# Optimization experiments

Measured on AMD Instinct MI355X. Metric: run time of the kernel, lower is better.

The kernel has to match this reference:

```python
import jax, jax.numpy as jnp
import numpy as np
from jax import lax

V, E, C_OUT, K, NTAGS = 32000, 256, 256, 3, 32
B, T = 64, 2048


def setup_inputs() -> dict:
    key = jax.random.key(0)
    ks = jax.random.split(key, 12)
    inputs = jax.random.randint(ks[0], (B, T), 0, V)
    emb_table = jax.random.normal(ks[1], (V, E), jnp.float32) * 0.02
    emb_table = emb_table.at[1].set(0.0)  # padding_idx=1
    conv1_w = jax.random.normal(ks[2], (C_OUT, E, K), jnp.float32) * 0.02
    conv1_b = jax.random.normal(ks[3], (C_OUT,), jnp.float32) * 0.02
    conv2_w = jax.random.normal(ks[4], (C_OUT, C_OUT, K), jnp.float32) * 0.02
    conv2_b = jax.random.normal(ks[5], (C_OUT,), jnp.float32) * 0.02
    fc_w = jax.random.normal(ks[6], (NTAGS, E), jnp.float32) * 0.02
    fc_b = jax.random.normal(ks[7], (NTAGS,), jnp.float32) * 0.02
    trans = jax.random.normal(ks[8], (NTAGS, NTAGS), jnp.float32) * 0.1
    start_t = jax.random.normal(ks[9], (NTAGS,), jnp.float32) * 0.1
    end_t = jax.random.normal(ks[10], (NTAGS,), jnp.float32) * 0.1
    return {"inputs": inputs, "emb_table": emb_table,
            "conv1_w": conv1_w, "conv1_b": conv1_b,
            "conv2_w": conv2_w, "conv2_b": conv2_b,
            "fc_w": fc_w, "fc_b": fc_b,
            "trans": trans, "start_t": start_t, "end_t": end_t}


def _conv1d(x, w, b):
    # x: [B, C_in, T], w: [C_out, C_in, K], padding=1
    y = lax.conv_general_dilated(x, w, window_strides=(1,), padding=[(1, 1)],
                                 dimension_numbers=("NCH", "OIH", "NCH"))
    return y + b[None, :, None]


def _crf_log_partition(emissions, trans, start_t, end_t):
    # emissions: [B, T, NTAGS] -> logZ per sequence [B]
    em_t = jnp.swapaxes(emissions, 0, 1)  # [T, B, NTAGS]
    alpha0 = start_t[None, :] + em_t[0]   # [B, NTAGS]

    def step(alpha, emit):
        # alpha: [B, C]; broadcast prev-tag x next-tag: [B, C, C]
        scores = alpha[:, :, None] + trans[None, :, :] + emit[:, None, :]
        new_alpha = jax.scipy.special.logsumexp(scores, axis=1)
        return new_alpha, None

    alpha, _ = lax.scan(step, alpha0, em_t[1:])
    return jax.scipy.special.logsumexp(alpha + end_t[None, :], axis=-1)


def reference(inputs, emb_table, conv1_w, conv1_b, conv2_w, conv2_b,
              fc_w, fc_b, trans, start_t, end_t):
    emb = emb_table[inputs]                    # [B, T, E]
    x = jnp.swapaxes(emb, 1, 2)                # [B, E, T]
    x = _conv1d(x, conv1_w, conv1_b)           # [B, C, T]
    x = _conv1d(x, conv2_w, conv2_b)           # [B, C, T]
    h = jnp.swapaxes(x, 1, 2)                  # [B, T, E]  (dropout = identity in eval)
    logits = jnp.einsum("bte,ce->btc", h, fc_w) + fc_b  # [B, T, NTAGS]
    return _crf_log_partition(logits, trans, start_t, end_t)  # [B]
```

## Files before the change

### kernel.cpp

```cpp
#include <hip/hip_runtime.h>
#include <hip/hip_bf16.h>

typedef float f32x4 __attribute__((ext_vector_type(4)));
typedef __bf16 bf16x8 __attribute__((ext_vector_type(8)));
typedef __bf16 bf16x4 __attribute__((ext_vector_type(4)));

__global__ __launch_bounds__(256) void transpose_w(const float* __restrict__ w1,
                                                   const float* __restrict__ w2,
                                                   float* __restrict__ w1t,
                                                   float* __restrict__ w2t) {
  int tid = blockIdx.x * 256 + threadIdx.x;
  if (tid < 196608) {
    float v = w1[tid];
    int k1 = tid % 3;
    int r = tid / 3;
    int e = r & 255;
    int cp = r >> 8;
    w1t[(k1 * 256 + e) * 256 + cp] = v;
  } else {
    int t2 = tid - 196608;
    float v = w2[t2];
    int k2 = t2 % 3;
    int r = t2 / 3;
    int cp = r & 255;
    int c = r >> 8;
    w2t[(k2 * 256 + cp) * 256 + c] = v;
  }
}

__global__ __launch_bounds__(256) void prep_g(const float* __restrict__ fcw,
                                              const float* __restrict__ w2t,
                                              float* __restrict__ G) {
  int tid = blockIdx.x * 256 + threadIdx.x;
  int cp = tid & 255;
  int rest = tid >> 8;
  int n = rest & 31;
  int k2 = rest >> 5;
  const float* wr = w2t + (k2 * 256 + cp) * 256;
  const float* fr = fcw + n * 256;
  float acc = 0.f;
  #pragma unroll 8
  for (int c = 0; c < 256; c += 4) {
    f32x4 a = *(const f32x4*)(fr + c);
    f32x4 bb = *(const f32x4*)(wr + c);
    acc = fmaf(a[0], bb[0], acc); acc = fmaf(a[1], bb[1], acc);
    acc = fmaf(a[2], bb[2], acc); acc = fmaf(a[3], bb[3], acc);
  }
  G[(k2 * 32 + n) * 256 + cp] = acc;
}

__global__ __launch_bounds__(256) void prep_wf(const float* __restrict__ G,
                                               const float* __restrict__ w1t,
                                               const float* __restrict__ b1,
                                               const float* __restrict__ b2,
                                               const float* __restrict__ fcw,
                                               const float* __restrict__ fcb,
                                               __bf16* __restrict__ wfb,
                                               float* __restrict__ C0,
                                               float* __restrict__ CT,
                                               float* __restrict__ bias_tot,
                                               float* __restrict__ c0v,
                                               float* __restrict__ cTv) {
  int tid = blockIdx.x * 256 + threadIdx.x;
  if (tid < 40960) {
    int n = tid & 31;
    int r = tid >> 5;
    int kk = r % 5;
    int e = r / 5;
    float acc = 0.f;
    #pragma unroll
    for (int k2 = 0; k2 < 3; ++k2) {
      int k1 = kk - k2;
      if (k1 < 0 || k1 > 2) continue;
      const float* g = G + (k2 * 32 + n) * 256;
      const float* wr = w1t + (k1 * 256 + e) * 256;
      #pragma unroll 8
      for (int cp = 0; cp < 256; cp += 4) {
        f32x4 a = *(const f32x4*)(g + cp);
        f32x4 bb = *(const f32x4*)(wr + cp);
        acc = fmaf(a[0], bb[0], acc); acc = fmaf(a[1], bb[1], acc);
        acc = fmaf(a[2], bb[2], acc); acc = fmaf(a[3], bb[3], acc);
      }
    }
    int j = kk * 32 + n;
    int jt = j >> 4, jl = j & 15;
    int et = e >> 5, el = e & 31;
    int lane = jl | ((el >> 3) << 4);
    int rr = el & 7;
    wfb[((jt * 8 + et) * 64 + lane) * 8 + rr] = (__bf16)acc;
  } else if (tid < 57344) {
    int t2 = tid - 40960;
    int which = (t2 >= 8192);
    if (which) t2 -= 8192;
    int n = t2 & 31;
    int e = t2 >> 5;
    const float* g = G + ((which ? 2 : 0) * 32 + n) * 256;
    int k1 = which ? 0 : 2;
    const float* wr = w1t + (k1 * 256 + e) * 256;
    float acc = 0.f;
    #pragma unroll 8
    for (int cp = 0; cp < 256; cp += 4) {
      f32x4 a = *(const f32x4*)(g + cp);
      f32x4 bb = *(const f32x4*)(wr + cp);
      acc = fmaf(a[0], bb[0], acc); acc = fmaf(a[1], bb[1], acc);
      acc = fmaf(a[2], bb[2], acc); acc = fmaf(a[3], bb[3], acc);
    }
    (which ? CT : C0)[n * 256 + e] = acc;
  } else if (tid < 57376) {
    int n = tid - 57344;
    float bt = fcb[n];
    for (int c = 0; c < 256; ++c) bt = fmaf(fcw[n * 256 + c], b2[c], bt);
    float s0 = 0.f, s1 = 0.f, s2 = 0.f;
    const float* g0 = G + (0 * 32 + n) * 256;
    const float* g1 = G + (1 * 32 + n) * 256;
    const float* g2 = G + (2 * 32 + n) * 256;
    for (int cp = 0; cp < 256; ++cp) {
      s0 = fmaf(g0[cp], b1[cp], s0);
      s1 = fmaf(g1[cp], b1[cp], s1);
      s2 = fmaf(g2[cp], b1[cp], s2);
    }
    bias_tot[n] = bt + s0 + s1 + s2;
    c0v[n] = s0;
    cTv[n] = s2;
  }
}

__global__ __launch_bounds__(256) void ptab_corr(const float* __restrict__ emb,
                                                 const __bf16* __restrict__ wfb,
                                                 __bf16* __restrict__ P,
                                                 const int* __restrict__ idx,
                                                 const float* __restrict__ C0,
                                                 const float* __restrict__ CT,
                                                 const float* __restrict__ c0v,
                                                 const float* __restrict__ cTv,
                                                 float* __restrict__ corr) {
  __shared__ float red[256];
  if (blockIdx.x < 500) {
    int lane = threadIdx.x & 63;
    int mt = blockIdx.x * 4 + (threadIdx.x >> 6);
    int ln = lane & 15;
    int q = lane >> 4;
    int m = mt * 16 + ln;
    f32x4 acc[10];
    #pragma unroll
    for (int jt = 0; jt < 10; ++jt) acc[jt] = (f32x4){0.f, 0.f, 0.f, 0.f};
    const float* arow = emb + m * 256 + q * 8;
    #pragma unroll
    for (int et = 0; et < 8; ++et) {
      f32x4 a0 = *(const f32x4*)(arow + et * 32);
      f32x4 a1 = *(const f32x4*)(arow + et * 32 + 4);
      bf16x8 af;
      af[0] = (__bf16)a0[0]; af[1] = (__bf16)a0[1];
      af[2] = (__bf16)a0[2]; af[3] = (__bf16)a0[3];
      af[4] = (__bf16)a1[0]; af[5] = (__bf16)a1[1];
      af[6] = (__bf16)a1[2]; af[7] = (__bf16)a1[3];
      #pragma unroll
      for (int jt = 0; jt < 10; ++jt) {
        bf16x8 bfr = *(const bf16x8*)(wfb + ((jt * 8 + et) * 64 + lane) * 8);
        acc[jt] = __builtin_amdgcn_mfma_f32_16x16x32_bf16(af, bfr, acc[jt], 0, 0, 0);
      }
    }
    #pragma unroll
    for (int jt = 0; jt < 10; ++jt) {
      __bf16* pp = P + (mt * 16 + q * 4) * 160 + jt * 16 + ln;
      pp[0]   = (__bf16)acc[jt][0];
      pp[160] = (__bf16)acc[jt][1];
      pp[320] = (__bf16)acc[jt][2];
      pp[480] = (__bf16)acc[jt][3];
    }
  } else {
    int bid = blockIdx.x - 500;
    int b = bid >> 1;
    int which = bid & 1;
    int n = threadIdx.x & 31;
    int part = threadIdx.x >> 5;
    int v = idx[b * 2048 + (which ? 2047 : 0)];
    const float* C = which ? CT : C0;
    const float* er = emb + v * 256 + part * 32;
    const float* cr = C + n * 256 + part * 32;
    float s = 0.f;
    #pragma unroll
    for (int e = 0; e < 32; ++e) s = fmaf(cr[e], er[e], s);
    red[threadIdx.x] = s;
    __syncthreads();
    if (part == 0) {
      float tot = (which ? cTv : c0v)[n];
      #pragma unroll
      for (int p = 0; p < 8; ++p) tot += red[p * 32 + n];
      corr[(which * 64 + b) * 32 + n] = tot;
    }
  }
}

__global__ __launch_bounds__(256) void logits_k(const int* __restrict__ idx,
                                                const __bf16* __restrict__ P,
                                                const float* __restrict__ bias_tot,
                                                const float* __restrict__ corr,
                                                __bf16* __restrict__ L) {
  int tid = blockIdx.x * 256 + threadIdx.x;
  int q = tid & 7;
  int tp = (tid >> 3) & 1023;
  int b = tid >> 13;
  int t0 = tp * 2;
  const int* ib = idx + b * 2048;
  f32x4 bias = *(const f32x4*)(bias_tot + q * 4);
  f32x4 acc0 = bias, acc1 = bias;
  #pragma unroll
  for (int j = 0; j < 6; ++j) {
    int tt = t0 + j - 2;
    if (tt < 0 || tt > 2047) continue;
    int v = ib[tt];
    const __bf16* pr = P + v * 160 + q * 4;
    if (j < 5) {
      bf16x4 pv = *(const bf16x4*)(pr + j * 32);
      acc0[0] += (float)pv[0]; acc0[1] += (float)pv[1];
      acc0[2] += (float)pv[2]; acc0[3] += (float)pv[3];
    }
    if (j >= 1) {
      bf16x4 pv = *(const bf16x4*)(pr + (j - 1) * 32);
      acc1[0] += (float)pv[0]; acc1[1] += (float)pv[1];
      acc1[2] += (float)pv[2]; acc1[3] += (float)pv[3];
    }
  }
  if (t0 == 0)        acc0 -= *(const f32x4*)(corr + b * 32 + q * 4);
  if (t0 + 1 == 2047) acc1 -= *(const f32x4*)(corr + (64 + b) * 32 + q * 4);
  bf16x4 r0, r1;
  r0[0] = (__bf16)(__expf(acc0[0]) * 0.03125f);
  r0[1] = (__bf16)(__expf(acc0[1]) * 0.03125f);
  r0[2] = (__bf16)(__expf(acc0[2]) * 0.03125f);
  r0[3] = (__bf16)(__expf(acc0[3]) * 0.03125f);
  r1[0] = (__bf16)(__expf(acc1[0]) * 0.03125f);
  r1[1] = (__bf16)(__expf(acc1[1]) * 0.03125f);
  r1[2] = (__bf16)(__expf(acc1[2]) * 0.03125f);
  r1[3] = (__bf16)(__expf(acc1[3]) * 0.03125f);
  __bf16* Lb = L + (b * 2048 + t0) * 32 + q * 4;
  *(bf16x4*)(Lb) = r0;
  *(bf16x4*)(Lb + 32) = r1;
}

__global__ __launch_bounds__(256) void crf_stage1(const __bf16* __restrict__ Lexp,
                                                  const float* __restrict__ trans,
                                                  __bf16* __restrict__ PcB) {
  __shared__ __bf16 sl[4][32 * 40];
  int lane = threadIdx.x & 63;
  int w = threadIdx.x >> 6;
  int chain = blockIdx.x * 4 + w;
  int c = chain >> 6;
  int b = chain & 63;
  int ln = lane & 15;
  int q = lane >> 4;
  float tA0[8], tA1[8];
  #pragma unroll
  for (int e = 0; e < 8; ++e) {
    tA0[e] = __expf(trans[(q * 8 + e) * 32 + ln]);
    tA1[e] = __expf(trans[(q * 8 + e) * 32 + 16 + ln]);
  }
  bf16x8 bf0, bf1;
  #pragma unroll
  for (int e = 0; e < 8; ++e) {
    int k = q * 8 + e;
    bf0[e] = (k == ln) ? (__bf16)1.0f : (__bf16)0.0f;
    bf1[e] = (k == 16 + ln) ? (__bf16)1.0f : (__bf16)0.0f;
  }
  int tstart = c * 32 + 1;
  int total = (c == 63) ? 31 : 32;
  const __bf16* Le = Lexp + (b * 2048 + tstart) * 32;
  __bf16* myS = &sl[w][0];

  auto step = [&](float sc0, float sc1) {
    bf16x8 a0, a1;
    #pragma unroll
    for (int e = 0; e < 8; ++e) {
      a0[e] = (__bf16)(sc0 * tA0[e]);
      a1[e] = (__bf16)(sc1 * tA1[e]);
    }
    f32x4 z = {0.f, 0.f, 0.f, 0.f};
    f32x4 c00 = __builtin_amdgcn_mfma_f32_16x16x32_bf16(a0, bf0, z, 0, 0, 0);
    f32x4 c01 = __builtin_amdgcn_mfma_f32_16x16x32_bf16(a0, bf1, z, 0, 0, 0);
    f32x4 c10 = __builtin_amdgcn_mfma_f32_16x16x32_bf16(a1, bf0, z, 0, 0, 0);
    f32x4 c11 = __builtin_amdgcn_mfma_f32_16x16x32_bf16(a1, bf1, z, 0, 0, 0);
    bf16x4 w00, w01, w10, w11;
    #pragma unroll
    for (int r = 0; r < 4; ++r) {
      w00[r] = (__bf16)c00[r]; w01[r] = (__bf16)c01[r];
      w10[r] = (__bf16)c10[r]; w11[r] = (__bf16)c11[r];
    }
    *(bf16x4*)(myS + (ln) * 40      + q * 4)      = w00;
    *(bf16x4*)(myS + (16 + ln) * 40 + q * 4)      = w01;
    *(bf16x4*)(myS + (ln) * 40      + 16 + q * 4) = w10;
    *(bf16x4*)(myS + (16 + ln) * 40 + 16 + q * 4) = w11;
    bf0 = *(const bf16x8*)(myS + (ln) * 40 + q * 8);
    bf1 = *(const bf16x8*)(myS + (16 + ln) * 40 + q * 8);
  };

  float s0[8], s1[8];
  #pragma unroll
  for (int i = 0; i < 8; ++i) {
    s0[i] = (float)Le[i * 32 + ln];
    s1[i] = (float)Le[i * 32 + 16 + ln];
  }
  int nbatch = total >> 3;
  int rem = total & 7;
  for (int bt = 0; bt < nbatch; ++bt) {
    float n0[8], n1[8];
    bool more = (bt + 1 < nbatch) || (rem != 0 && bt + 1 == nbatch);
    if (more) {
      int bs = (bt + 1) * 8;
      #pragma unroll
      for (int i = 0; i < 8; ++i) {
        int k = bs + i; if (k >= total) k = total - 1;
        n0[i] = (float)Le[k * 32 + ln];
        n1[i] = (float)Le[k * 32 + 16 + ln];
      }
    }
    #pragma unroll
    for (int s = 0; s < 8; ++s) step(s0[s], s1[s]);
    #pragma unroll
    for (int i = 0; i < 8; ++i) { s0[i] = n0[i]; s1[i] = n1[i]; }
  }
  if (rem) {
    #pragma unroll
    for (int s = 0; s < 7; ++s) step(s0[s], s1[s]);
  }
  bf16x8 o0, o1;
  #pragma unroll
  for (int e = 0; e < 8; ++e) {
    o0[e] = myS[(q * 8 + e) * 40 + ln];
    o1[e] = myS[(q * 8 + e) * 40 + 16 + ln];
  }
  __bf16* dst = PcB + ((b * 64 + c) * 64 + lane) * 16;
  *(bf16x8*)(dst)     = o0;
  *(bf16x8*)(dst + 8) = o1;
}

__global__ __launch_bounds__(512) void crf_tail(const __bf16* __restrict__ Lexp,
                                                const __bf16* __restrict__ PcB,
                                                const float* __restrict__ start_t,
                                                const float* __restrict__ end_t,
                                                float* __restrict__ out) {
  __shared__ float sg[8][1024];
  __shared__ __bf16 sl[8][32 * 40];
  int b = blockIdx.x;
  int tid = threadIdx.x;
  int lane = tid & 63;
  int g = tid >> 6;
  int ln = lane & 15;
  int q = lane >> 4;
  const __bf16* base = PcB + ((b * 64 + g * 8) * 64) * 16;
  bf16x8 a0 = *(const bf16x8*)(base + lane * 16);
  bf16x8 a1 = *(const bf16x8*)(base + lane * 16 + 8);
  bf16x8 bf0, bf1;
  #pragma unroll
  for (int e = 0; e < 8; ++e) {
    int k = q * 8 + e;
    bf0[e] = (k == ln) ? (__bf16)1.0f : (__bf16)0.0f;
    bf1[e] = (k == 16 + ln) ? (__bf16)1.0f : (__bf16)0.0f;
  }
  __bf16* myS = &sl[g][0];
  f32x4 c00, c01, c10, c11;
  for (int j = 0; j < 8; ++j) {
    bf16x8 na0, na1;
    if (j < 7) {
      const __bf16* nb = base + (j + 1) * 1024 + lane * 16;
      na0 = *(const bf16x8*)(nb);
      na1 = *(const bf16x8*)(nb + 8);
    }
    f32x4 z = {0.f, 0.f, 0.f, 0.f};
    c00 = __builtin_amdgcn_mfma_f32_16x16x32_bf16(a0, bf0, z, 0, 0, 0);
    c01 = __builtin_amdgcn_mfma_f32_16x16x32_bf16(a0, bf1, z, 0, 0, 0);
    c10 = __builtin_amdgcn_mfma_f32_16x16x32_bf16(a1, bf0, z, 0, 0, 0);
    c11 = __builtin_amdgcn_mfma_f32_16x16x32_bf16(a1, bf1, z, 0, 0, 0);
    if (j < 7) {
      bf16x4 w00, w01, w10, w11;
      #pragma unroll
      for (int r = 0; r < 4; ++r) {
        w00[r] = (__bf16)c00[r]; w01[r] = (__bf16)c01[r];
        w10[r] = (__bf16)c10[r]; w11[r] = (__bf16)c11[r];
      }
      *(bf16x4*)(myS + (ln) * 40      + q * 4)      = w00;
      *(bf16x4*)(myS + (16 + ln) * 40 + q * 4)      = w01;
      *(bf16x4*)(myS + (ln) * 40      + 16 + q * 4) = w10;
      *(bf16x4*)(myS + (16 + ln) * 40 + 16 + q * 4) = w11;
      bf0 = *(const bf16x8*)(myS + (ln) * 40 + q * 8);
      bf1 = *(const bf16x8*)(myS + (16 + ln) * 40 + q * 8);
      a0 = na0; a1 = na1;
    }
  }
  #pragma unroll
  for (int r = 0; r < 4; ++r) {
    sg[g][(ln) * 32      + q * 4 + r]      = c00[r];
    sg[g][(16 + ln) * 32 + q * 4 + r]      = c01[r];
    sg[g][(ln) * 32      + 16 + q * 4 + r] = c10[r];
    sg[g][(16 + ln) * 32 + 16 + q * 4 + r] = c11[r];
  }
  int j2 = tid & 31;
  float u = __expf(start_t[j2]) * (float)Lexp[b * 2048 * 32 + j2] * 32.f;
  __syncthreads();
  float logacc = 0.f;
  #pragma unroll
  for (int gg = 0; gg < 8; ++gg) {
    const float* M = &sg[gg][0];
    float nu0 = 0.f, nu1 = 0.f, nu2 = 0.f, nu3 = 0.f;
    #pragma unroll
    for (int k = 0; k < 32; k += 4) {
      nu0 = fmaf(__shfl(u, k,     32), M[(k)     * 32 + j2], nu0);
      nu1 = fmaf(__shfl(u, k + 1, 32), M[(k + 1) * 32 + j2], nu1);
      nu2 = fmaf(__shfl(u, k + 2, 32), M[(k + 2) * 32 + j2], nu2);
      nu3 = fmaf(__shfl(u, k + 3, 32), M[(k + 3) * 32 + j2], nu3);
    }
    float nu = (nu0 + nu1) + (nu2 + nu3);
    float ssum = nu;
    #pragma unroll
    for (int o = 1; o < 32; o <<= 1) ssum += __shfl_xor(ssum, o, 32);
    u = nu * __builtin_amdgcn_rcpf(ssum);
    logacc += __logf(ssum);
  }
  float term = u * __expf(end_t[j2]);
  #pragma unroll
  for (int o = 1; o < 32; o <<= 1) term += __shfl_xor(term, o, 32);
  if (tid == 0)
    out[b] = logacc + logf(term) + (float)(2047.0 * 5.0 * 0.69314718055994530942);
}

extern "C" void kernel_launch(void* const* d_in, const int* in_sizes, int n_in,
                              void* d_out, int out_size, void* d_ws, size_t ws_size,
                              hipStream_t stream) {
  const int*   idx  = (const int*)d_in[0];
  const float* emb  = (const float*)d_in[1];
  const float* w1   = (const float*)d_in[2];
  const float* b1   = (const float*)d_in[3];
  const float* w2   = (const float*)d_in[4];
  const float* b2   = (const float*)d_in[5];
  const float* fcw  = (const float*)d_in[6];
  const float* fcb  = (const float*)d_in[7];
  const float* trn  = (const float*)d_in[8];
  const float* st   = (const float*)d_in[9];
  const float* en   = (const float*)d_in[10];

  char* ws = (char*)d_ws;
  __bf16* P     = (__bf16*)(ws + 0);
  __bf16* L     = (__bf16*)(ws + 10240000);
  __bf16* PcB   = (__bf16*)(ws + 18628608);
  float*  w1t   = (float*)(ws + 27017216);
  float*  w2t   = (float*)(ws + 27803648);
  __bf16* WfB   = (__bf16*)(ws + 43794432);
  float*  G     = (float*)(ws + 43876352);
  float*  C0    = (float*)(ws + 43974656);
  float*  CT    = (float*)(ws + 44007424);
  float*  bias  = (float*)(ws + 44040192);
  float*  c0v   = (float*)(ws + 44040320);
  float*  cTv   = (float*)(ws + 44040448);
  float*  corr  = (float*)(ws + 44040576);

  transpose_w<<<1536, 256, 0, stream>>>(w1, w2, w1t, w2t);
  prep_g     <<<96,   256, 0, stream>>>(fcw, w2t, G);
  prep_wf    <<<225,  256, 0, stream>>>(G, w1t, b1, b2, fcw, fcb, WfB, C0, CT, bias, c0v, cTv);
  ptab_corr  <<<628,  256, 0, stream>>>(emb, WfB, P, idx, C0, CT, c0v, cTv, corr);
  logits_k   <<<2048, 256, 0, stream>>>(idx, P, bias, corr, L);
  crf_stage1 <<<1024, 256, 0, stream>>>(L, trn, PcB);
  crf_tail   <<<64,   512, 0, stream>>>(L, PcB, st, en, (float*)d_out);
}
```

Measured before the change: 186.6 us.

## Drop weight transpose kernel; stage raw conv weights in shared memory for prep

Removes the separate transpose_w kernel and its w1t/w2t workspace buffers. prep_g and prep_wf now load slices of the original conv weights straight into LDS and compute from there, with two accumulators per dot product. This saves one launch and the global round-trip of transposed weights. The cost is far fewer blocks (32 instead of 96/225), so the prep kernels have much less parallelism, and the bias block is serialized onto block 0.

```diff
diff --git a/kernel.cpp b/kernel.cpp
--- a/kernel.cpp
+++ b/kernel.cpp
@@ -5,52 +5,37 @@
 typedef __bf16 bf16x8 __attribute__((ext_vector_type(8)));
 typedef __bf16 bf16x4 __attribute__((ext_vector_type(4)));
 
-__global__ __launch_bounds__(256) void transpose_w(const float* __restrict__ w1,
-                                                   const float* __restrict__ w2,
-                                                   float* __restrict__ w1t,
-                                                   float* __restrict__ w2t) {
-  int tid = blockIdx.x * 256 + threadIdx.x;
-  if (tid < 196608) {
-    float v = w1[tid];
-    int k1 = tid % 3;
-    int r = tid / 3;
-    int e = r & 255;
-    int cp = r >> 8;
-    w1t[(k1 * 256 + e) * 256 + cp] = v;
-  } else {
-    int t2 = tid - 196608;
-    float v = w2[t2];
-    int k2 = t2 % 3;
-    int r = t2 / 3;
-    int cp = r & 255;
-    int c = r >> 8;
-    w2t[(k2 * 256 + cp) * 256 + c] = v;
-  }
-}
-
 __global__ __launch_bounds__(256) void prep_g(const float* __restrict__ fcw,
-                                              const float* __restrict__ w2t,
+                                              const float* __restrict__ w2,
                                               float* __restrict__ G) {
-  int tid = blockIdx.x * 256 + threadIdx.x;
-  int cp = tid & 255;
-  int rest = tid >> 8;
-  int n = rest & 31;
-  int k2 = rest >> 5;
-  const float* wr = w2t + (k2 * 256 + cp) * 256;
-  const float* fr = fcw + n * 256;
-  float acc = 0.f;
-  #pragma unroll 8
-  for (int c = 0; c < 256; c += 4) {
-    f32x4 a = *(const f32x4*)(fr + c);
-    f32x4 bb = *(const f32x4*)(wr + c);
-    acc = fmaf(a[0], bb[0], acc); acc = fmaf(a[1], bb[1], acc);
-    acc = fmaf(a[2], bb[2], acc); acc = fmaf(a[3], bb[3], acc);
-  }
-  G[(k2 * 32 + n) * 256 + cp] = acc;
+  __shared__ float s[256 * 24];
+  int cp0 = blockIdx.x * 8;
+  for (int l = threadIdx.x; l < 256 * 24; l += 256) {
+    int c = l / 24, r = l - c * 24;
+    s[l] = w2[c * 768 + cp0 * 3 + r];
+  }
+  __syncthreads();
+  #pragma unroll
+  for (int o = 0; o < 3; ++o) {
+    int oid = threadIdx.x + o * 256;
+    int cpl = oid & 7;
+    int p = oid >> 3;
+    int n = p & 31, k2 = p >> 5;
+    const float* fr = fcw + n * 256;
+    float a0 = 0.f, a1 = 0.f;
+    for (int c = 0; c < 256; c += 4) {
+      f32x4 a = *(const f32x4*)(fr + c);
+      a0 = fmaf(a[0], s[(c + 0) * 24 + cpl * 3 + k2], a0);
+      a1 = fmaf(a[1], s[(c + 1) * 24 + cpl * 3 + k2], a1);
+      a0 = fmaf(a[2], s[(c + 2) * 24 + cpl * 3 + k2], a0);
+      a1 = fmaf(a[3], s[(c + 3) * 24 + cpl * 3 + k2], a1);
+    }
+    G[(k2 * 32 + n) * 256 + cp0 + cpl] = a0 + a1;
+  }
 }
 
 __global__ __launch_bounds__(256) void prep_wf(const float* __restrict__ G,
-                                               const float* __restrict__ w1t,
+                                               const float* __restrict__ w1,
                                                const float* __restrict__ b1,
                                                const float* __restrict__ b2,
                                                const float* __restrict__ fcw,
@@ -61,53 +46,65 @@
                                                float* __restrict__ bias_tot,
                                                float* __restrict__ c0v,
                                                float* __restrict__ cTv) {
-  int tid = blockIdx.x * 256 + threadIdx.x;
-  if (tid < 40960) {
-    int n = tid & 31;
-    int r = tid >> 5;
-    int kk = r % 5;
-    int e = r / 5;
+  __shared__ float s[256 * 24];
+  int e0 = blockIdx.x * 8;
+  for (int l = threadIdx.x; l < 256 * 24; l += 256) {
+    int cp = l / 24, r = l - cp * 24;
+    s[l] = w1[cp * 768 + e0 * 3 + r];
+  }
+  __syncthreads();
+  #pragma unroll
+  for (int o = 0; o < 5; ++o) {
+    int oid = threadIdx.x + o * 256;
+    int el = oid / 160;
+    int rem = oid - el * 160;
+    int kk = rem >> 5;
+    int n = rem & 31;
+    int e = e0 + el;
     float acc = 0.f;
     #pragma unroll
     for (int k2 = 0; k2 < 3; ++k2) {
       int k1 = kk - k2;
       if (k1 < 0 || k1 > 2) continue;
       const float* g = G + (k2 * 32 + n) * 256;
-      const float* wr = w1t + (k1 * 256 + e) * 256;
-      #pragma unroll 8
+      float a0 = 0.f, a1 = 0.f;
       for (int cp = 0; cp < 256; cp += 4) {
-        f32x4 a = *(const f32x4*)(g + cp);
-        f32x4 bb = *(const f32x4*)(wr + cp);
-        acc = fmaf(a[0], bb[0], acc); acc = fmaf(a[1], bb[1], acc);
-        acc = fmaf(a[2], bb[2], acc); acc = fmaf(a[3], bb[3], acc);
+        f32x4 gv = *(const f32x4*)(g + cp);
+        a0 = fmaf(gv[0], s[(cp + 0) * 24 + el * 3 + k1], a0);
+        a1 = fmaf(gv[1], s[(cp + 1) * 24 + el * 3 + k1], a1);
+        a0 = fmaf(gv[2], s[(cp + 2) * 24 + el * 3 + k1], a0);
+        a1 = fmaf(gv[3], s[(cp + 3) * 24 + el * 3 + k1], a1);
       }
+      acc += a0 + a1;
     }
     int j = kk * 32 + n;
     int jt = j >> 4, jl = j & 15;
-    int et = e >> 5, el = e & 31;
-    int lane = jl | ((el >> 3) << 4);
-    int rr = el & 7;
+    int et = e >> 5, el2 = e & 31;
+    int lane = jl | ((el2 >> 3) << 4);
+    int rr = el2 & 7;
     wfb[((jt * 8 + et) * 64 + lane) * 8 + rr] = (__bf16)acc;
-  } else if (tid < 57344) {
-    int t2 = tid - 40960;
-    int which = (t2 >= 8192);
-    if (which) t2 -= 8192;
-    int n = t2 & 31;
-    int e = t2 >> 5;
+  }
+  #pragma unroll
+  for (int o = 0; o < 2; ++o) {
+    int oid = threadIdx.x + o * 256;
+    int which = oid >> 8;
+    int el = (oid >> 5) & 7;
+    int n = oid & 31;
+    int e = e0 + el;
+    int k1 = which ? 0 : 2;
     const float* g = G + ((which ? 2 : 0) * 32 + n) * 256;
-    int k1 = which ? 0 : 2;
-    const float* wr = w1t + (k1 * 256 + e) * 256;
-    float acc = 0.f;
-    #pragma unroll 8
+    float a0 = 0.f, a1 = 0.f;
     for (int cp = 0; cp < 256; cp += 4) {
-      f32x4 a = *(const f32x4*)(g + cp);
-      f32x4 bb = *(const f32x4*)(wr + cp);
-      acc = fmaf(a[0], bb[0], acc); acc = fmaf(a[1], bb[1], acc);
-      acc = fmaf(a[2], bb[2], acc); acc = fmaf(a[3], bb[3], acc);
-    }
-    (which ? CT : C0)[n * 256 + e] = acc;
-  } else if (tid < 57376) {
-    int n = tid - 57344;
+      f32x4 gv = *(const f32x4*)(g + cp);
+      a0 = fmaf(gv[0], s[(cp + 0) * 24 + el * 3 + k1], a0);
+      a1 = fmaf(gv[1], s[(cp + 1) * 24 + el * 3 + k1], a1);
+      a0 = fmaf(gv[2], s[(cp + 2) * 24 + el * 3 + k1], a0);
+      a1 = fmaf(gv[3], s[(cp + 3) * 24 + el * 3 + k1], a1);
+    }
+    (which ? CT : C0)[n * 256 + e] = a0 + a1;
+  }
+  if (blockIdx.x == 0 && threadIdx.x < 32) {
+    int n = threadIdx.x;
     float bt = fcb[n];
     for (int c = 0; c < 256; ++c) bt = fmaf(fcw[n * 256 + c], b2[c], bt);
     float s0 = 0.f, s1 = 0.f, s2 = 0.f;
@@ -441,22 +438,19 @@
   __bf16* P     = (__bf16*)(ws + 0);
   __bf16* L     = (__bf16*)(ws + 10240000);
   __bf16* PcB   = (__bf16*)(ws + 18628608);
-  float*  w1t   = (float*)(ws + 27017216);
-  float*  w2t   = (float*)(ws + 27803648);
-  __bf16* WfB   = (__bf16*)(ws + 43794432);
-  float*  G     = (float*)(ws + 43876352);
-  float*  C0    = (float*)(ws + 43974656);
-  float*  CT    = (float*)(ws + 44007424);
-  float*  bias  = (float*)(ws + 44040192);
-  float*  c0v   = (float*)(ws + 44040320);
-  float*  cTv   = (float*)(ws + 44040448);
-  float*  corr  = (float*)(ws + 44040576);
-
-  transpose_w<<<1536, 256, 0, stream>>>(w1, w2, w1t, w2t);
-  prep_g     <<<96,   256, 0, stream>>>(fcw, w2t, G);
-  prep_wf    <<<225,  256, 0, stream>>>(G, w1t, b1, b2, fcw, fcb, WfB, C0, CT, bias, c0v, cTv);
-  ptab_corr  <<<628,  256, 0, stream>>>(emb, WfB, P, idx, C0, CT, c0v, cTv, corr);
-  logits_k   <<<2048, 256, 0, stream>>>(idx, P, bias, corr, L);
-  crf_stage1 <<<1024, 256, 0, stream>>>(L, trn, PcB);
-  crf_tail   <<<64,   512, 0, stream>>>(L, PcB, st, en, (float*)d_out);
-}
+  __bf16* WfB   = (__bf16*)(ws + 27017216);
+  float*  G     = (float*)(ws + 27099136);
+  float*  C0    = (float*)(ws + 27197440);
+  float*  CT    = (float*)(ws + 27230208);
+  float*  bias  = (float*)(ws + 27262976);
+  float*  c0v   = (float*)(ws + 27263104);
+  float*  cTv   = (float*)(ws + 27263232);
+  float*  corr  = (float*)(ws + 27263360);
+
+  prep_g    <<<32,   256, 0, stream>>>(fcw, w2, G);
+  prep_wf   <<<32,   256, 0, stream>>>(G, w1, b1, b2, fcw, fcb, WfB, C0, CT, bias, c0v, cTv);
+  ptab_corr <<<628,  256, 0, stream>>>(emb, WfB, P, idx, C0, CT, c0v, cTv, corr);
+  logits_k  <<<2048, 256, 0, stream>>>(idx, P, bias, corr, L);
+  crf_stage1<<<1024, 256, 0, stream>>>(L, trn, PcB);
+  crf_tail  <<<64,   512, 0, stream>>>(L, PcB, st, en, (float*)d_out);
+}
```

Result: slower. 254.6 us (+36.4%).

## Fuse CRF tail into stage1 via last-block atomic counter per sequence

Applied to the files above, without the earlier changes.

Removes the separate crf_tail launch. Each crf_stage1 block now bumps a per-sequence atomic counter after writing its chunk products, and the block that finishes last for a sequence combines that sequence's chunk matrices and computes the final log-partition. The counters are zeroed in prep_g, and workspace offsets are compacted to make room for them. This saves a kernel launch and the tail's serial dependency on the whole stage, at the cost of threadfence/atomic overhead and the combine matrices being held in bf16 instead of fp32 in shared memory.

```diff
diff --git a/kernel.cpp b/kernel.cpp
--- a/kernel.cpp
+++ b/kernel.cpp
@@ -30,7 +30,9 @@
 
 __global__ __launch_bounds__(256) void prep_g(const float* __restrict__ fcw,
                                               const float* __restrict__ w2t,
-                                              float* __restrict__ G) {
+                                              float* __restrict__ G,
+                                              int* __restrict__ cnt) {
+  if (blockIdx.x == 0 && threadIdx.x < 64) cnt[threadIdx.x] = 0;
   int tid = blockIdx.x * 256 + threadIdx.x;
   int cp = tid & 255;
   int rest = tid >> 8;
@@ -240,8 +242,14 @@
 
 __global__ __launch_bounds__(256) void crf_stage1(const __bf16* __restrict__ Lexp,
                                                   const float* __restrict__ trans,
-                                                  __bf16* __restrict__ PcB) {
+                                                  __bf16* __restrict__ PcB,
+                                                  const float* __restrict__ start_t,
+                                                  const float* __restrict__ end_t,
+                                                  int* __restrict__ cnt,
+                                                  float* __restrict__ out) {
   __shared__ __bf16 sl[4][32 * 40];
+  __shared__ __bf16 sgB[8][1024];
+  __shared__ int winb[4];
   int lane = threadIdx.x & 63;
   int w = threadIdx.x >> 6;
   int chain = blockIdx.x * 4 + w;
@@ -331,95 +339,102 @@
   __bf16* dst = PcB + ((b * 64 + c) * 64 + lane) * 16;
   *(bf16x8*)(dst)     = o0;
   *(bf16x8*)(dst + 8) = o1;
-}
-
-__global__ __launch_bounds__(512) void crf_tail(const __bf16* __restrict__ Lexp,
-                                                const __bf16* __restrict__ PcB,
-                                                const float* __restrict__ start_t,
-                                                const float* __restrict__ end_t,
-                                                float* __restrict__ out) {
-  __shared__ float sg[8][1024];
-  __shared__ __bf16 sl[8][32 * 40];
-  int b = blockIdx.x;
-  int tid = threadIdx.x;
-  int lane = tid & 63;
-  int g = tid >> 6;
-  int ln = lane & 15;
-  int q = lane >> 4;
-  const __bf16* base = PcB + ((b * 64 + g * 8) * 64) * 16;
-  bf16x8 a0 = *(const bf16x8*)(base + lane * 16);
-  bf16x8 a1 = *(const bf16x8*)(base + lane * 16 + 8);
-  bf16x8 bf0, bf1;
-  #pragma unroll
-  for (int e = 0; e < 8; ++e) {
-    int k = q * 8 + e;
-    bf0[e] = (k == ln) ? (__bf16)1.0f : (__bf16)0.0f;
-    bf1[e] = (k == 16 + ln) ? (__bf16)1.0f : (__bf16)0.0f;
-  }
-  __bf16* myS = &sl[g][0];
-  f32x4 c00, c01, c10, c11;
-  for (int j = 0; j < 8; ++j) {
-    bf16x8 na0, na1;
-    if (j < 7) {
-      const __bf16* nb = base + (j + 1) * 1024 + lane * 16;
-      na0 = *(const bf16x8*)(nb);
-      na1 = *(const bf16x8*)(nb + 8);
-    }
-    f32x4 z = {0.f, 0.f, 0.f, 0.f};
-    c00 = __builtin_amdgcn_mfma_f32_16x16x32_bf16(a0, bf0, z, 0, 0, 0);
-    c01 = __builtin_amdgcn_mfma_f32_16x16x32_bf16(a0, bf1, z, 0, 0, 0);
-    c10 = __builtin_amdgcn_mfma_f32_16x16x32_bf16(a1, bf0, z, 0, 0, 0);
-    c11 = __builtin_amdgcn_mfma_f32_16x16x32_bf16(a1, bf1, z, 0, 0, 0);
-    if (j < 7) {
-      bf16x4 w00, w01, w10, w11;
+
+  __threadfence();
+  __syncthreads();
+  if (threadIdx.x < 4) {
+    int myb = ((blockIdx.x * 4) & 63) + threadIdx.x;
+    int old = atomicAdd(&cnt[myb], 1);
+    winb[threadIdx.x] = (old == 63) ? myb : -1;
+  }
+  __syncthreads();
+
+  for (int s = 0; s < 4; ++s) {
+    int wb = winb[s];
+    if (wb < 0) continue;
+    __threadfence();
+    #pragma unroll
+    for (int half = 0; half < 2; ++half) {
+      int g = w + half * 4;
+      const __bf16* base = PcB + ((wb * 64 + g * 8) * 64) * 16;
+      bf16x8 a0 = *(const bf16x8*)(base + lane * 16);
+      bf16x8 a1 = *(const bf16x8*)(base + lane * 16 + 8);
+      bf16x8 tb0, tb1;
+      #pragma unroll
+      for (int e = 0; e < 8; ++e) {
+        int k = q * 8 + e;
+        tb0[e] = (k == ln) ? (__bf16)1.0f : (__bf16)0.0f;
+        tb1[e] = (k == 16 + ln) ? (__bf16)1.0f : (__bf16)0.0f;
+      }
+      f32x4 d00, d01, d10, d11;
+      for (int j = 0; j < 8; ++j) {
+        bf16x8 na0, na1;
+        if (j < 7) {
+          const __bf16* nb = base + (j + 1) * 1024 + lane * 16;
+          na0 = *(const bf16x8*)(nb);
+          na1 = *(const bf16x8*)(nb + 8);
+        }
+        f32x4 z = {0.f, 0.f, 0.f, 0.f};
+        d00 = __builtin_amdgcn_mfma_f32_16x16x32_bf16(a0, tb0, z, 0, 0, 0);
+        d01 = __builtin_amdgcn_mfma_f32_16x16x32_bf16(a0, tb1, z, 0, 0, 0);
+        d10 = __builtin_amdgcn_mfma_f32_16x16x32_bf16(a1, tb0, z, 0, 0, 0);
+        d11 = __builtin_amdgcn_mfma_f32_16x16x32_bf16(a1, tb1, z, 0, 0, 0);
+        if (j < 7) {
+          bf16x4 w00, w01, w10, w11;
+          #pragma unroll
+          for (int r = 0; r < 4; ++r) {
+            w00[r] = (__bf16)d00[r]; w01[r] = (__bf16)d01[r];
+            w10[r] = (__bf16)d10[r]; w11[r] = (__bf16)d11[r];
+          }
+          *(bf16x4*)(myS + (ln) * 40      + q * 4)      = w00;
+          *(bf16x4*)(myS + (16 + ln) * 40 + q * 4)      = w01;
+          *(bf16x4*)(myS + (ln) * 40      + 16 + q * 4) = w10;
+          *(bf16x4*)(myS + (16 + ln) * 40 + 16 + q * 4) = w11;
+          tb0 = *(const bf16x8*)(myS + (ln) * 40 + q * 8);
+          tb1 = *(const bf16x8*)(myS + (16 + ln) * 40 + q * 8);
+          a0 = na0; a1 = na1;
+        }
+      }
+      bf16x4 m00, m01, m10, m11;
       #pragma unroll
       for (int r = 0; r < 4; ++r) {
-        w00[r] = (__bf16)c00[r]; w01[r] = (__bf16)c01[r];
-        w10[r] = (__bf16)c10[r]; w11[r] = (__bf16)c11[r];
-      }
-      *(bf16x4*)(myS + (ln) * 40      + q * 4)      = w00;
-      *(bf16x4*)(myS + (16 + ln) * 40 + q * 4)      = w01;
-      *(bf16x4*)(myS + (ln) * 40      + 16 + q * 4) = w10;
-      *(bf16x4*)(myS + (16 + ln) * 40 + 16 + q * 4) = w11;
-      bf0 = *(const bf16x8*)(myS + (ln) * 40 + q * 8);
-      bf1 = *(const bf16x8*)(myS + (16 + ln) * 40 + q * 8);
-      a0 = na0; a1 = na1;
-    }
-  }
-  #pragma unroll
-  for (int r = 0; r < 4; ++r) {
-    sg[g][(ln) * 32      + q * 4 + r]      = c00[r];
-    sg[g][(16 + ln) * 32 + q * 4 + r]      = c01[r];
-    sg[g][(ln) * 32      + 16 + q * 4 + r] = c10[r];
-    sg[g][(16 + ln) * 32 + 16 + q * 4 + r] = c11[r];
-  }
-  int j2 = tid & 31;
-  float u = __expf(start_t[j2]) * (float)Lexp[b * 2048 * 32 + j2] * 32.f;
-  __syncthreads();
-  float logacc = 0.f;
-  #pragma unroll
-  for (int gg = 0; gg < 8; ++gg) {
-    const float* M = &sg[gg][0];
-    float nu0 = 0.f, nu1 = 0.f, nu2 = 0.f, nu3 = 0.f;
-    #pragma unroll
-    for (int k = 0; k < 32; k += 4) {
-      nu0 = fmaf(__shfl(u, k,     32), M[(k)     * 32 + j2], nu0);
-      nu1 = fmaf(__shfl(u, k + 1, 32), M[(k + 1) * 32 + j2], nu1);
-      nu2 = fmaf(__shfl(u, k + 2, 32), M[(k + 2) * 32 + j2], nu2);
-      nu3 = fmaf(__shfl(u, k + 3, 32), M[(k + 3) * 32 + j2], nu3);
-    }
-    float nu = (nu0 + nu1) + (nu2 + nu3);
-    float ssum = nu;
-    #pragma unroll
-    for (int o = 1; o < 32; o <<= 1) ssum += __shfl_xor(ssum, o, 32);
-    u = nu * __builtin_amdgcn_rcpf(ssum);
-    logacc += __logf(ssum);
-  }
-  float term = u * __expf(end_t[j2]);
-  #pragma unroll
-  for (int o = 1; o < 32; o <<= 1) term += __shfl_xor(term, o, 32);
-  if (tid == 0)
-    out[b] = logacc + logf(term) + (float)(2047.0 * 5.0 * 0.69314718055994530942);
+        m00[r] = (__bf16)d00[r]; m01[r] = (__bf16)d01[r];
+        m10[r] = (__bf16)d10[r]; m11[r] = (__bf16)d11[r];
+      }
+      *(bf16x4*)(&sgB[g][(ln) * 32      + q * 4])      = m00;
+      *(bf16x4*)(&sgB[g][(16 + ln) * 32 + q * 4])      = m01;
+      *(bf16x4*)(&sgB[g][(ln) * 32      + 16 + q * 4]) = m10;
+      *(bf16x4*)(&sgB[g][(16 + ln) * 32 + 16 + q * 4]) = m11;
+    }
+    __syncthreads();
+    int j2 = threadIdx.x & 31;
+    float u = __expf(start_t[j2]) * (float)Lexp[wb * 2048 * 32 + j2] * 32.f;
+    float logacc = 0.f;
+    #pragma unroll
+    for (int gg = 0; gg < 8; ++gg) {
+      const __bf16* M = &sgB[gg][0];
+      float nu0 = 0.f, nu1 = 0.f, nu2 = 0.f, nu3 = 0.f;
+      #pragma unroll
+      for (int k = 0; k < 32; k += 4) {
+        nu0 = fmaf(__shfl(u, k,     32), (float)M[(k)     * 32 + j2], nu0);
+        nu1 = fmaf(__shfl(u, k + 1, 32), (float)M[(k + 1) * 32 + j2], nu1);
+        nu2 = fmaf(__shfl(u, k + 2, 32), (float)M[(k + 2) * 32 + j2], nu2);
+        nu3 = fmaf(__shfl(u, k + 3, 32), (float)M[(k + 3) * 32 + j2], nu3);
+      }
+      float nu = (nu0 + nu1) + (nu2 + nu3);
+      float ssum = nu;
+      #pragma unroll
+      for (int o = 1; o < 32; o <<= 1) ssum += __shfl_xor(ssum, o, 32);
+      u = nu * __builtin_amdgcn_rcpf(ssum);
+      logacc += __logf(ssum);
+    }
+    float term = u * __expf(end_t[j2]);
+    #pragma unroll
+    for (int o = 1; o < 32; o <<= 1) term += __shfl_xor(term, o, 32);
+    if (threadIdx.x == 0)
+      out[wb] = logacc + logf(term) + (float)(2047.0 * 5.0 * 0.69314718055994530942);
+    __syncthreads();
+  }
 }
 
 extern "C" void kernel_launch(void* const* d_in, const int* in_sizes, int n_in,
@@ -443,20 +458,20 @@
   __bf16* PcB   = (__bf16*)(ws + 18628608);
   float*  w1t   = (float*)(ws + 27017216);
   float*  w2t   = (float*)(ws + 27803648);
-  __bf16* WfB   = (__bf16*)(ws + 43794432);
-  float*  G     = (float*)(ws + 43876352);
-  float*  C0    = (float*)(ws + 43974656);
-  float*  CT    = (float*)(ws + 44007424);
-  float*  bias  = (float*)(ws + 44040192);
-  float*  c0v   = (float*)(ws + 44040320);
-  float*  cTv   = (float*)(ws + 44040448);
-  float*  corr  = (float*)(ws + 44040576);
+  __bf16* WfB   = (__bf16*)(ws + 28590080);
+  float*  G     = (float*)(ws + 28672000);
+  float*  C0    = (float*)(ws + 28770304);
+  float*  CT    = (float*)(ws + 28803072);
+  float*  bias  = (float*)(ws + 28835840);
+  float*  c0v   = (float*)(ws + 28835968);
+  float*  cTv   = (float*)(ws + 28836096);
+  float*  corr  = (float*)(ws + 28836224);
+  int*    cnt   = (int*)(ws + 28852608);
 
   transpose_w<<<1536, 256, 0, stream>>>(w1, w2, w1t, w2t);
-  prep_g     <<<96,   256, 0, stream>>>(fcw, w2t, G);
+  prep_g     <<<96,   256, 0, stream>>>(fcw, w2t, G, cnt);
   prep_wf    <<<225,  256, 0, stream>>>(G, w1t, b1, b2, fcw, fcb, WfB, C0, CT, bias, c0v, cTv);
   ptab_corr  <<<628,  256, 0, stream>>>(emb, WfB, P, idx, C0, CT, c0v, cTv, corr);
   logits_k   <<<2048, 256, 0, stream>>>(idx, P, bias, corr, L);
-  crf_stage1 <<<1024, 256, 0, stream>>>(L, trn, PcB);
-  crf_tail   <<<64,   512, 0, stream>>>(L, PcB, st, en, (float*)d_out);
-}
+  crf_stage1 <<<1024, 256, 0, stream>>>(L, trn, PcB, st, en, cnt, (float*)d_out);
+}
```

Result: slower. 329.7 us (+76.6%).
